# Kernel optimization log

Measured on AMD Instinct MI355X. Metric: run time of the kernel, lower is better.

The kernel has to match this reference:

```python
import jax, jax.numpy as jnp
import numpy as np

H = 56; W = 56; WS = 7; SHIFT = 3; HEADS = 6; C = 192
HD = C // HEADS; N = WS * WS; NWH = H // WS; NWW = W // WS; NW = NWH * NWW
MLP_HID = 4 * C
EPS = 1e-5


def _rel_index(ws):
    coords = np.stack(np.meshgrid(np.arange(ws), np.arange(ws), indexing='ij'))  # [2,ws,ws]
    cf = coords.reshape(2, -1)                       # [2,N]
    rc = (cf[:, :, None] - cf[:, None, :]).transpose(1, 2, 0).astype(np.int64)  # [N,N,2]
    rc[..., 0] += ws - 1
    rc[..., 1] += ws - 1
    rc[..., 0] *= 2 * ws - 1
    return rc.sum(-1)                                # [N,N]


def _attn_mask(h, w, ws, shift):
    img = np.zeros((h, w), dtype=np.float32)
    slices = (slice(0, -ws), slice(-ws, -shift), slice(-shift, None))
    cnt = 0
    for hs in slices:
        for wsl in slices:
            img[hs, wsl] = cnt
            cnt += 1
    mw = img.reshape(h // ws, ws, w // ws, ws).transpose(0, 2, 1, 3).reshape(-1, ws * ws)  # [nW,N]
    am = mw[:, None, :] - mw[:, :, None]             # [nW,N,N] (unsqueeze(1)-unsqueeze(2))
    return np.where(am != 0, np.float32(-100.0), np.float32(0.0))


REL_IDX = jnp.asarray(_rel_index(WS))
ATTN_MASK = jnp.asarray(_attn_mask(H, W, WS, SHIFT))


def _ln(x, w, b):
    m = jnp.mean(x, axis=-1, keepdims=True)
    v = jnp.mean((x - m) ** 2, axis=-1, keepdims=True)
    return (x - m) * jax.lax.rsqrt(v + EPS) * w + b


def setup_inputs() -> dict:
    key = jax.random.key(0)
    ks = jax.random.split(key, 8)
    B = 64
    s = 0.02
    return {
        'x': jax.random.normal(ks[0], (B, H * W, C), jnp.float32),
        'norm1_w': jnp.ones((C,), jnp.float32),
        'norm1_b': jnp.zeros((C,), jnp.float32),
        'qkv_w': jax.random.normal(ks[1], (C, 3 * C), jnp.float32) * s,
        'qkv_b': jnp.zeros((3 * C,), jnp.float32),
        'proj_w': jax.random.normal(ks[2], (C, C), jnp.float32) * s,
        'proj_b': jnp.zeros((C,), jnp.float32),
        'rel_bias': jax.random.normal(ks[3], ((2 * WS - 1) ** 2, HEADS), jnp.float32) * s,
        'norm2_w': jnp.ones((C,), jnp.float32),
        'norm2_b': jnp.zeros((C,), jnp.float32),
        'fc1_w': jax.random.normal(ks[4], (C, MLP_HID), jnp.float32) * s,
        'fc1_b': jnp.zeros((MLP_HID,), jnp.float32),
        'fc2_w': jax.random.normal(ks[5], (MLP_HID, C), jnp.float32) * s,
        'fc2_b': jnp.zeros((C,), jnp.float32),
    }


def reference(x, norm1_w, norm1_b, qkv_w, qkv_b, proj_w, proj_b, rel_bias,
              norm2_w, norm2_b, fc1_w, fc1_b, fc2_w, fc2_b):
    B = x.shape[0]
    shortcut = x
    h = _ln(x, norm1_w, norm1_b).reshape(B, H, W, C)
    h = jnp.roll(h, (-SHIFT, -SHIFT), axis=(1, 2))
    # window partition -> [B*nW, N, C]
    wx = h.reshape(B, NWH, WS, NWW, WS, C).transpose(0, 1, 3, 2, 4, 5).reshape(B * NW, N, C)
    qkv = (wx @ qkv_w + qkv_b).reshape(B * NW, N, 3, HEADS, HD).transpose(2, 0, 3, 1, 4)
    q, k, v = qkv[0], qkv[1], qkv[2]                 # [BnW, heads, N, hd]
    attn = jnp.einsum('bhnd,bhmd->bhnm', q, k) * (HD ** -0.5)
    bias = rel_bias[REL_IDX.reshape(-1)].reshape(N, N, HEADS).transpose(2, 0, 1)  # [heads,N,N]
    attn = attn + bias[None]
    attn = attn.reshape(B, NW, HEADS, N, N) + ATTN_MASK[None, :, None]
    attn = jax.nn.softmax(attn.reshape(B * NW, HEADS, N, N), axis=-1)
    out = jnp.einsum('bhnm,bhmd->bhnd', attn, v).transpose(0, 2, 1, 3).reshape(B * NW, N, C)
    out = out @ proj_w + proj_b
    # window reverse -> [B,H,W,C]
    out = out.reshape(B, NWH, NWW, WS, WS, C).transpose(0, 1, 3, 2, 4, 5).reshape(B, H, W, C)
    out = jnp.roll(out, (SHIFT, SHIFT), axis=(1, 2)).reshape(B, H * W, C)
    x = shortcut + out
    h2 = _ln(x, norm2_w, norm2_b)
    h2 = jax.nn.gelu(h2 @ fc1_w + fc1_b, approximate=False)
    h2 = h2 @ fc2_w + fc2_b
    return x + h2
```

## Files before the change

kernel.cpp:

```cpp
#include <hip/hip_runtime.h>
#include <hip/hip_bf16.h>
#include <math.h>

typedef __bf16 bf16;
typedef bf16  bf16x4 __attribute__((ext_vector_type(4)));
typedef bf16  bf16x8 __attribute__((ext_vector_type(8)));
typedef float f32x4  __attribute__((ext_vector_type(4)));

#define CD 192
#define NHEADS 6

__device__ __forceinline__ bf16x8 ld_frag(const bf16* p, int r0, int k0, int ld) {
  const int l = threadIdx.x & 63;
  return *reinterpret_cast<const bf16x8*>(p + (r0 + (l & 15)) * ld + (k0 + 8 * (l >> 4)));
}

__device__ __forceinline__ f32x4 mfma16(bf16x8 a, bf16x8 b, f32x4 c) {
  return __builtin_amdgcn_mfma_f32_16x16x32_bf16(a, b, c, 0, 0, 0);
}

__device__ __forceinline__ float gelu_f(float v) {
  const float e = __expf(-1.5957691216057308f * (v + 0.044715f * v * v * v));
  return v * __builtin_amdgcn_rcpf(1.f + e);
}

__global__ void prep_pack(const float* __restrict__ src, bf16* __restrict__ dst, int K, int N) {
  const int t = blockIdx.x * 256 + threadIdx.x;
  const int ktiles = K >> 5;
  const int total = (N >> 4) * ktiles * 64;
  if (t >= total) return;
  const int l  = t & 63;
  const int r  = t >> 6;
  const int kt = r % ktiles;
  const int ng = r / ktiles;
  const int n  = ng * 16 + (l & 15);
  const int k0 = kt * 32 + 8 * (l >> 4);
  bf16x8 v;
  #pragma unroll
  for (int j = 0; j < 8; ++j) v[j] = (bf16)src[(size_t)(k0 + j) * N + n];
  *(reinterpret_cast<bf16x8*>(dst) + t) = v;
}

__global__ void prep_bm(const float* __restrict__ relb, float* __restrict__ bm) {
  const int idx = blockIdx.x * 256 + threadIdx.x;
  if (idx >= 4 * 6 * 64 * 64) return;
  const int k = idx & 63;
  const int r = (idx >> 6) & 63;
  const int h = (idx >> 12) % 6;
  const int c = idx / (4096 * 6);
  float v = -3000.f;
  if (r < 49 && k < 49) {
    const int rh = r / 7, rw = r % 7, kh = k / 7, kw = k % 7;
    const int crh = (c & 2) ? (rh < 4 ? 1 : 2) : 0;
    const int crw = (c & 1) ? (rw < 4 ? 1 : 2) : 0;
    const int ckh = (c & 2) ? (kh < 4 ? 1 : 2) : 0;
    const int ckw = (c & 1) ? (kw < 4 ? 1 : 2) : 0;
    const float mask = (crh == ckh && crw == ckw) ? 0.f : -100.f;
    v = relb[((rh - kh + 6) * 13 + (rw - kw + 6)) * 6 + h] + mask;
  }
  bm[idx] = v;
}

__global__ __launch_bounds__(768, 1)
void swin_attn_kernel(const float* __restrict__ x,
                      const float* __restrict__ n1w, const float* __restrict__ n1b,
                      const bf16* __restrict__ wqf, const float* __restrict__ qkvb,
                      const bf16* __restrict__ wpf, const float* __restrict__ projb,
                      const float* __restrict__ bm,
                      float* __restrict__ out)
{
  __shared__ alignas(16) bf16 sQ[NHEADS][64 * 40];
  __shared__ alignas(16) bf16 sK[NHEADS][64 * 40];
  __shared__ alignas(16) bf16 sVT[NHEADS][32 * 72];
  __shared__ alignas(16) bf16 sU[NHEADS * 64 * 72];

  const int l    = threadIdx.x & 63;
  const int wv   = threadIdx.x >> 6;
  const int h    = wv >> 1;
  const int half = wv & 1;
  const int r0w  = half * 32;
  const int b  = blockIdx.x >> 6;
  const int wi = blockIdx.x & 63;
  const int wh = wi >> 3, ww = wi & 7;
  const int cw = ((wh == 7) ? 2 : 0) + ((ww == 7) ? 1 : 0);

  bf16* sA = sU;

  float xv0[5], xv1[5], xv2[5];
  size_t basea[5];
  {
    #pragma unroll
    for (int it = 0; it < 5; ++it) {
      const int t = wv + it * 12;
      if (t < 49) {
        const int th = t / 7, tw = t - 7 * th;
        const int ho = (wh * 7 + th + 3) % 56;
        const int wo = (ww * 7 + tw + 3) % 56;
        const size_t base = ((size_t)b * 3136 + ho * 56 + wo) * CD;
        basea[it] = base;
        xv0[it] = x[base + l]; xv1[it] = x[base + l + 64]; xv2[it] = x[base + l + 128];
      }
    }
    const float w0 = n1w[l], w1 = n1w[l + 64], w2 = n1w[l + 128];
    const float c0 = n1b[l], c1 = n1b[l + 64], c2 = n1b[l + 128];
    #pragma unroll
    for (int it = 0; it < 5; ++it) {
      const int t = wv + it * 12;
      if (t < 49) {
        const float v0 = xv0[it], v1 = xv1[it], v2 = xv2[it];
        float s  = v0 + v1 + v2;
        float ss = v0 * v0 + v1 * v1 + v2 * v2;
        #pragma unroll
        for (int off = 32; off; off >>= 1) { s += __shfl_xor(s, off); ss += __shfl_xor(ss, off); }
        const float mean = s * (1.f / 192.f);
        const float inv  = rsqrtf(ss * (1.f / 192.f) - mean * mean + 1e-5f);
        sA[t * 200 + l]       = (bf16)((v0 - mean) * inv * w0 + c0);
        sA[t * 200 + l + 64]  = (bf16)((v1 - mean) * inv * w1 + c1);
        sA[t * 200 + l + 128] = (bf16)((v2 - mean) * inv * w2 + c2);
      }
    }
    for (int i = threadIdx.x; i < 15 * 200; i += 768) sA[49 * 200 + i] = (bf16)0.f;
  }
  __syncthreads();

  float bmreg[2][4][4];
  {
    const float* bmb = bm + ((size_t)(cw * 6 + h) << 12) + (l & 15);
    #pragma unroll
    for (int mt = 0; mt < 2; ++mt)
      #pragma unroll
      for (int i = 0; i < 4; ++i) {
        const int r = r0w + mt * 16 + (l >> 4) * 4 + i;
        #pragma unroll
        for (int nt = 0; nt < 4; ++nt)
          bmreg[mt][i][nt] = bmb[r * 64 + nt * 16];
      }
  }

  {
    const bf16x8* bq = reinterpret_cast<const bf16x8*>(wqf) + l;
    const int cs = wv;
    f32x4 acc[3][4] = {};
    #pragma unroll
    for (int ks = 0; ks < 6; ++ks) {
      const int k0 = ks * 32;
      bf16x8 af[4];
      #pragma unroll
      for (int mt = 0; mt < 4; ++mt) af[mt] = ld_frag(sA, mt * 16, k0, 200);
      #pragma unroll
      for (int nt = 0; nt < 3; ++nt) {
        const bf16x8 bfr = bq[((cs * 3 + nt) * 6 + ks) * 64];
        #pragma unroll
        for (int mt = 0; mt < 4; ++mt) acc[nt][mt] = mfma16(af[mt], bfr, acc[nt][mt]);
      }
    }
    #pragma unroll
    for (int nt = 0; nt < 3; ++nt) {
      const int col0 = cs * 48 + nt * 16;
      const int which = col0 / 192;
      const int rem   = col0 - which * 192;
      const int hh    = rem >> 5;
      const int cc    = (rem & 31) + (l & 15);
      const float bias = qkvb[col0 + (l & 15)];
      #pragma unroll
      for (int mt = 0; mt < 4; ++mt) {
        const int rb = mt * 16 + (l >> 4) * 4;
        if (which == 2) {
          bf16x4 pv;
          #pragma unroll
          for (int i = 0; i < 4; ++i) pv[i] = (bf16)(acc[nt][mt][i] + bias);
          *reinterpret_cast<bf16x4*>(&sVT[hh][cc * 72 + rb]) = pv;
        } else if (which == 0) {
          #pragma unroll
          for (int i = 0; i < 4; ++i)
            sQ[hh][(rb + i) * 40 + cc] = (bf16)((acc[nt][mt][i] + bias) * 0.17677669529663689f);
        } else {
          #pragma unroll
          for (int i = 0; i < 4; ++i)
            sK[hh][(rb + i) * 40 + cc] = (bf16)(acc[nt][mt][i] + bias);
        }
      }
    }
  }
  __syncthreads();

  bf16* sP = sU + h * (64 * 72);
  {
    f32x4 sc[2][4] = {};
    bf16x8 qf0 = ld_frag(sQ[h], r0w,      0, 40);
    bf16x8 qf1 = ld_frag(sQ[h], r0w + 16, 0, 40);
    #pragma unroll
    for (int nt = 0; nt < 4; ++nt) {
      const bf16x8 kf = ld_frag(sK[h], nt * 16, 0, 40);
      sc[0][nt] = mfma16(qf0, kf, sc[0][nt]);
      sc[1][nt] = mfma16(qf1, kf, sc[1][nt]);
    }
    #pragma unroll
    for (int mt = 0; mt < 2; ++mt)
      #pragma unroll
      for (int i = 0; i < 4; ++i) {
        const int r = r0w + mt * 16 + (l >> 4) * 4 + i;
        float p[4], sum = 0.f;
        #pragma unroll
        for (int nt = 0; nt < 4; ++nt) {
          p[nt] = __expf(sc[mt][nt][i] + bmreg[mt][i][nt]);
          sum += p[nt];
        }
        #pragma unroll
        for (int off = 1; off < 16; off <<= 1) sum += __shfl_xor(sum, off);
        const float isum = __builtin_amdgcn_rcpf(sum);
        #pragma unroll
        for (int nt = 0; nt < 4; ++nt)
          sP[r * 72 + nt * 16 + (l & 15)] = (bf16)(p[nt] * isum);
      }
  }

  f32x4 o[2][2] = {};
  #pragma unroll
  for (int ks = 0; ks < 2; ++ks) {
    const int k0 = ks * 32;
    bf16x8 pf0 = ld_frag(sP, r0w,      k0, 72);
    bf16x8 pf1 = ld_frag(sP, r0w + 16, k0, 72);
    #pragma unroll
    for (int nt = 0; nt < 2; ++nt) {
      const bf16x8 vf = ld_frag(sVT[h], nt * 16, k0, 72);
      o[0][nt] = mfma16(pf0, vf, o[0][nt]);
      o[1][nt] = mfma16(pf1, vf, o[1][nt]);
    }
  }
  __syncthreads();
  {
    bf16* sAO = sU;
    #pragma unroll
    for (int nt = 0; nt < 2; ++nt) {
      const int c = h * 32 + nt * 16 + (l & 15);
      #pragma unroll
      for (int mt = 0; mt < 2; ++mt)
        #pragma unroll
        for (int i = 0; i < 4; ++i) {
          const int r = r0w + mt * 16 + (l >> 4) * 4 + i;
          sAO[r * 200 + c] = (bf16)o[mt][nt][i];
        }
    }
  }
  __syncthreads();

  f32x4 po[4] = {};
  {
    const bf16* sAO = sU;
    const bf16x8* bp = reinterpret_cast<const bf16x8*>(wpf) + l;
    #pragma unroll
    for (int ks = 0; ks < 6; ++ks) {
      const int k0 = ks * 32;
      const bf16x8 bfr = bp[(wv * 6 + ks) * 64];
      #pragma unroll
      for (int mt = 0; mt < 4; ++mt) {
        bf16x8 af = ld_frag(sAO, mt * 16, k0, 200);
        po[mt] = mfma16(af, bfr, po[mt]);
      }
    }
  }
  {
    bf16* sPO = &sVT[0][0];
    const int c = wv * 16 + (l & 15);
    const float bias = projb[c];
    #pragma unroll
    for (int mt = 0; mt < 4; ++mt)
      #pragma unroll
      for (int i = 0; i < 4; ++i) {
        const int r = mt * 16 + (l >> 4) * 4 + i;
        sPO[r * 200 + c] = (bf16)(po[mt][i] + bias);
      }
  }
  __syncthreads();

  {
    const bf16* sPO = &sVT[0][0];
    #pragma unroll
    for (int it = 0; it < 5; ++it) {
      const int r = wv + it * 12;
      if (r < 49) {
        const size_t base = basea[it];
        out[base + l]       = (float)sPO[r * 200 + l]       + xv0[it];
        out[base + l + 64]  = (float)sPO[r * 200 + l + 64]  + xv1[it];
        out[base + l + 128] = (float)sPO[r * 200 + l + 128] + xv2[it];
      }
    }
  }
}

__global__ __launch_bounds__(512, 6)
void swin_mlp_kernel(const float* __restrict__ n2w, const float* __restrict__ n2b,
                     const bf16* __restrict__ w1f, const float* __restrict__ fb1,
                     const bf16* __restrict__ w2f, const float* __restrict__ fb2,
                     float* __restrict__ io)
{
  __shared__ alignas(16) bf16 sA[64 * 200];
  __shared__ alignas(16) bf16 sH[2][64 * 72];
  const int l  = threadIdx.x & 63;
  const int wv = threadIdx.x >> 6;
  const int wr = wv & 1;
  const int wc = wv >> 1;
  const size_t t0 = (size_t)blockIdx.x * 64;

  {
    const float w0 = n2w[l], w1 = n2w[l + 64], w2 = n2w[l + 128];
    const float c0 = n2b[l], c1 = n2b[l + 64], c2 = n2b[l + 128];
    for (int t = wv; t < 64; t += 8) {
      const float* xr = io + (t0 + t) * CD;
      float v0 = xr[l], v1 = xr[l + 64], v2 = xr[l + 128];
      float s  = v0 + v1 + v2;
      float ss = v0 * v0 + v1 * v1 + v2 * v2;
      #pragma unroll
      for (int off = 32; off; off >>= 1) { s += __shfl_xor(s, off); ss += __shfl_xor(ss, off); }
      const float mean = s * (1.f / 192.f);
      const float inv  = rsqrtf(ss * (1.f / 192.f) - mean * mean + 1e-5f);
      sA[t * 200 + l]       = (bf16)((v0 - mean) * inv * w0 + c0);
      sA[t * 200 + l + 64]  = (bf16)((v1 - mean) * inv * w1 + c1);
      sA[t * 200 + l + 128] = (bf16)((v2 - mean) * inv * w2 + c2);
    }
  }
  __syncthreads();

  f32x4 oacc[2][3] = {};
  const bf16x8* w1p = reinterpret_cast<const bf16x8*>(w1f) + l;
  const bf16x8* w2p = reinterpret_cast<const bf16x8*>(w2f) + l;

  for (int kc = 0; kc < 12; ++kc) {
    bf16* hb = sH[kc & 1];
    f32x4 acc[2] = {};
    {
      bf16x8 b1[6];
      const bf16x8* b1p = w1p + ((kc * 4 + wc) * 6) * 64;
      #pragma unroll
      for (int ks = 0; ks < 6; ++ks) b1[ks] = b1p[ks * 64];

      #pragma unroll
      for (int ks = 0; ks < 6; ++ks) {
        const int k0 = ks * 32;
        bf16x8 af0 = ld_frag(sA, wr * 32,      k0, 200);
        bf16x8 af1 = ld_frag(sA, wr * 32 + 16, k0, 200);
        acc[0] = mfma16(af0, b1[ks], acc[0]);
        acc[1] = mfma16(af1, b1[ks], acc[1]);
      }
    }

    bf16x8 b2[6];
    #pragma unroll
    for (int ks = 0; ks < 2; ++ks)
      #pragma unroll
      for (int nt = 0; nt < 3; ++nt)
        b2[ks * 3 + nt] = w2p[((wc * 3 + nt) * 24 + kc * 2 + ks) * 64];

    {
      const int col = wc * 16 + (l & 15);
      const float bias = fb1[kc * 64 + col];
      #pragma unroll
      for (int mt = 0; mt < 2; ++mt)
        #pragma unroll
        for (int i = 0; i < 4; ++i) {
          const int r = wr * 32 + mt * 16 + (l >> 4) * 4 + i;
          hb[r * 72 + col] = (bf16)gelu_f(acc[mt][i] + bias);
        }
    }
    __syncthreads();
    #pragma unroll
    for (int ks = 0; ks < 2; ++ks) {
      const int k0 = ks * 32;
      bf16x8 af0 = ld_frag(hb, wr * 32,      k0, 72);
      bf16x8 af1 = ld_frag(hb, wr * 32 + 16, k0, 72);
      #pragma unroll
      for (int nt = 0; nt < 3; ++nt) {
        oacc[0][nt] = mfma16(af0, b2[ks * 3 + nt], oacc[0][nt]);
        oacc[1][nt] = mfma16(af1, b2[ks * 3 + nt], oacc[1][nt]);
      }
    }
  }

  #pragma unroll
  for (int nt = 0; nt < 3; ++nt) {
    const int col = wc * 48 + nt * 16 + (l & 15);
    const float bias = fb2[col];
    #pragma unroll
    for (int mt = 0; mt < 2; ++mt)
      #pragma unroll
      for (int i = 0; i < 4; ++i) {
        const int r = wr * 32 + mt * 16 + (l >> 4) * 4 + i;
        const size_t idx = (t0 + r) * CD + col;
        __builtin_nontemporal_store(oacc[mt][nt][i] + bias + io[idx], &io[idx]);
      }
  }
}

extern "C" void kernel_launch(void* const* d_in, const int* in_sizes, int n_in,
                              void* d_out, int out_size, void* d_ws, size_t ws_size,
                              hipStream_t stream) {
  const float* x     = (const float*)d_in[0];
  const float* n1w   = (const float*)d_in[1];
  const float* n1b   = (const float*)d_in[2];
  const float* qkvw  = (const float*)d_in[3];
  const float* qkvb  = (const float*)d_in[4];
  const float* projw = (const float*)d_in[5];
  const float* projb = (const float*)d_in[6];
  const float* relb  = (const float*)d_in[7];
  const float* n2w   = (const float*)d_in[8];
  const float* n2b   = (const float*)d_in[9];
  const float* f1w   = (const float*)d_in[10];
  const float* f1b   = (const float*)d_in[11];
  const float* f2w   = (const float*)d_in[12];
  const float* f2b   = (const float*)d_in[13];

  char* ws = (char*)d_ws;
  bf16*  wqf = (bf16*)(ws + 0);
  bf16*  wpf = (bf16*)(ws + 221184);
  bf16*  w1f = (bf16*)(ws + 294912);
  bf16*  w2f = (bf16*)(ws + 589824);
  float* bm  = (float*)(ws + 884736);

  prep_pack<<<(36 * 6 * 64 + 255) / 256, 256, 0, stream>>>(qkvw, wqf, 192, 576);
  prep_pack<<<(12 * 6 * 64 + 255) / 256, 256, 0, stream>>>(projw, wpf, 192, 192);
  prep_pack<<<(48 * 6 * 64 + 255) / 256, 256, 0, stream>>>(f1w, w1f, 192, 768);
  prep_pack<<<(12 * 24 * 64 + 255) / 256, 256, 0, stream>>>(f2w, w2f, 768, 192);
  prep_bm<<<(4 * 6 * 64 * 64 + 255) / 256, 256, 0, stream>>>(relb, bm);

  swin_attn_kernel<<<4096, 768, 0, stream>>>(x, n1w, n1b, wqf, qkvb, wpf, projb, bm, (float*)d_out);
  swin_mlp_kernel<<<3136, 512, 0, stream>>>(n2w, n2b, w1f, f1b, w2f, f2b, (float*)d_out);
}
```

Baseline: 470.1 us.

## Process two windows per attention block and prefetch both windows' inputs up front

New measurement: 814.9 us. 73.3% more time.

```diff
diff --git a/kernel.cpp b/kernel.cpp
--- a/kernel.cpp
+++ b/kernel.cpp
@@ -79,16 +79,20 @@
   const int h    = wv >> 1;
   const int half = wv & 1;
   const int r0w  = half * 32;
-  const int b  = blockIdx.x >> 6;
-  const int wi = blockIdx.x & 63;
-  const int wh = wi >> 3, ww = wi & 7;
-  const int cw = ((wh == 7) ? 2 : 0) + ((ww == 7) ? 1 : 0);
 
   bf16* sA = sU;
 
-  float xv0[5], xv1[5], xv2[5];
-  size_t basea[5];
-  {
+  int whA[2], wwA[2], cwA[2];
+  float xv0[2][5], xv1[2][5], xv2[2][5];
+  size_t basea[2][5];
+  #pragma unroll
+  for (int w2 = 0; w2 < 2; ++w2) {
+    const int w  = blockIdx.x * 2 + w2;
+    const int b  = w >> 6;
+    const int wi = w & 63;
+    const int wh = wi >> 3, ww = wi & 7;
+    whA[w2] = wh; wwA[w2] = ww;
+    cwA[w2] = ((wh == 7) ? 2 : 0) + ((ww == 7) ? 1 : 0);
     #pragma unroll
     for (int it = 0; it < 5; ++it) {
       const int t = wv + it * 12;
@@ -97,17 +101,27 @@
         const int ho = (wh * 7 + th + 3) % 56;
         const int wo = (ww * 7 + tw + 3) % 56;
         const size_t base = ((size_t)b * 3136 + ho * 56 + wo) * CD;
-        basea[it] = base;
-        xv0[it] = x[base + l]; xv1[it] = x[base + l + 64]; xv2[it] = x[base + l + 128];
-      }
-    }
-    const float w0 = n1w[l], w1 = n1w[l + 64], w2 = n1w[l + 128];
-    const float c0 = n1b[l], c1 = n1b[l + 64], c2 = n1b[l + 128];
+        basea[w2][it] = base;
+        xv0[w2][it] = x[base + l];
+        xv1[w2][it] = x[base + l + 64];
+        xv2[w2][it] = x[base + l + 128];
+      }
+    }
+  }
+
+  const float w0 = n1w[l], w1 = n1w[l + 64], w2c = n1w[l + 128];
+  const float c0 = n1b[l], c1 = n1b[l + 64], c2 = n1b[l + 128];
+  const bf16x8* bq = reinterpret_cast<const bf16x8*>(wqf) + l;
+  const bf16x8* bp = reinterpret_cast<const bf16x8*>(wpf) + l;
+
+  for (int w2 = 0; w2 < 2; ++w2) {
+    const int cw = cwA[w2];
+
     #pragma unroll
     for (int it = 0; it < 5; ++it) {
       const int t = wv + it * 12;
       if (t < 49) {
-        const float v0 = xv0[it], v1 = xv1[it], v2 = xv2[it];
+        const float v0 = xv0[w2][it], v1 = xv1[w2][it], v2 = xv2[w2][it];
         float s  = v0 + v1 + v2;
         float ss = v0 * v0 + v1 * v1 + v2 * v2;
         #pragma unroll
@@ -116,174 +130,172 @@
         const float inv  = rsqrtf(ss * (1.f / 192.f) - mean * mean + 1e-5f);
         sA[t * 200 + l]       = (bf16)((v0 - mean) * inv * w0 + c0);
         sA[t * 200 + l + 64]  = (bf16)((v1 - mean) * inv * w1 + c1);
-        sA[t * 200 + l + 128] = (bf16)((v2 - mean) * inv * w2 + c2);
+        sA[t * 200 + l + 128] = (bf16)((v2 - mean) * inv * w2c + c2);
       }
     }
     for (int i = threadIdx.x; i < 15 * 200; i += 768) sA[49 * 200 + i] = (bf16)0.f;
-  }
-  __syncthreads();
-
-  float bmreg[2][4][4];
-  {
-    const float* bmb = bm + ((size_t)(cw * 6 + h) << 12) + (l & 15);
-    #pragma unroll
-    for (int mt = 0; mt < 2; ++mt)
-      #pragma unroll
-      for (int i = 0; i < 4; ++i) {
-        const int r = r0w + mt * 16 + (l >> 4) * 4 + i;
-        #pragma unroll
-        for (int nt = 0; nt < 4; ++nt)
-          bmreg[mt][i][nt] = bmb[r * 64 + nt * 16];
-      }
-  }
-
-  {
-    const bf16x8* bq = reinterpret_cast<const bf16x8*>(wqf) + l;
-    const int cs = wv;
-    f32x4 acc[3][4] = {};
-    #pragma unroll
-    for (int ks = 0; ks < 6; ++ks) {
-      const int k0 = ks * 32;
-      bf16x8 af[4];
-      #pragma unroll
-      for (int mt = 0; mt < 4; ++mt) af[mt] = ld_frag(sA, mt * 16, k0, 200);
-      #pragma unroll
-      for (int nt = 0; nt < 3; ++nt) {
-        const bf16x8 bfr = bq[((cs * 3 + nt) * 6 + ks) * 64];
-        #pragma unroll
-        for (int mt = 0; mt < 4; ++mt) acc[nt][mt] = mfma16(af[mt], bfr, acc[nt][mt]);
-      }
-    }
-    #pragma unroll
-    for (int nt = 0; nt < 3; ++nt) {
-      const int col0 = cs * 48 + nt * 16;
-      const int which = col0 / 192;
-      const int rem   = col0 - which * 192;
-      const int hh    = rem >> 5;
-      const int cc    = (rem & 31) + (l & 15);
-      const float bias = qkvb[col0 + (l & 15)];
-      #pragma unroll
-      for (int mt = 0; mt < 4; ++mt) {
-        const int rb = mt * 16 + (l >> 4) * 4;
-        if (which == 2) {
-          bf16x4 pv;
-          #pragma unroll
-          for (int i = 0; i < 4; ++i) pv[i] = (bf16)(acc[nt][mt][i] + bias);
-          *reinterpret_cast<bf16x4*>(&sVT[hh][cc * 72 + rb]) = pv;
-        } else if (which == 0) {
-          #pragma unroll
-          for (int i = 0; i < 4; ++i)
-            sQ[hh][(rb + i) * 40 + cc] = (bf16)((acc[nt][mt][i] + bias) * 0.17677669529663689f);
-        } else {
-          #pragma unroll
-          for (int i = 0; i < 4; ++i)
-            sK[hh][(rb + i) * 40 + cc] = (bf16)(acc[nt][mt][i] + bias);
-        }
-      }
-    }
-  }
-  __syncthreads();
-
-  bf16* sP = sU + h * (64 * 72);
-  {
-    f32x4 sc[2][4] = {};
-    bf16x8 qf0 = ld_frag(sQ[h], r0w,      0, 40);
-    bf16x8 qf1 = ld_frag(sQ[h], r0w + 16, 0, 40);
-    #pragma unroll
-    for (int nt = 0; nt < 4; ++nt) {
-      const bf16x8 kf = ld_frag(sK[h], nt * 16, 0, 40);
-      sc[0][nt] = mfma16(qf0, kf, sc[0][nt]);
-      sc[1][nt] = mfma16(qf1, kf, sc[1][nt]);
-    }
-    #pragma unroll
-    for (int mt = 0; mt < 2; ++mt)
-      #pragma unroll
-      for (int i = 0; i < 4; ++i) {
-        const int r = r0w + mt * 16 + (l >> 4) * 4 + i;
-        float p[4], sum = 0.f;
-        #pragma unroll
-        for (int nt = 0; nt < 4; ++nt) {
-          p[nt] = __expf(sc[mt][nt][i] + bmreg[mt][i][nt]);
-          sum += p[nt];
-        }
-        #pragma unroll
-        for (int off = 1; off < 16; off <<= 1) sum += __shfl_xor(sum, off);
-        const float isum = __builtin_amdgcn_rcpf(sum);
-        #pragma unroll
-        for (int nt = 0; nt < 4; ++nt)
-          sP[r * 72 + nt * 16 + (l & 15)] = (bf16)(p[nt] * isum);
-      }
-  }
-
-  f32x4 o[2][2] = {};
-  #pragma unroll
-  for (int ks = 0; ks < 2; ++ks) {
-    const int k0 = ks * 32;
-    bf16x8 pf0 = ld_frag(sP, r0w,      k0, 72);
-    bf16x8 pf1 = ld_frag(sP, r0w + 16, k0, 72);
-    #pragma unroll
-    for (int nt = 0; nt < 2; ++nt) {
-      const bf16x8 vf = ld_frag(sVT[h], nt * 16, k0, 72);
-      o[0][nt] = mfma16(pf0, vf, o[0][nt]);
-      o[1][nt] = mfma16(pf1, vf, o[1][nt]);
-    }
-  }
-  __syncthreads();
-  {
-    bf16* sAO = sU;
-    #pragma unroll
-    for (int nt = 0; nt < 2; ++nt) {
-      const int c = h * 32 + nt * 16 + (l & 15);
+    __syncthreads();
+
+    float bmreg[2][4][4];
+    {
+      const float* bmb = bm + ((size_t)(cw * 6 + h) << 12) + (l & 15);
       #pragma unroll
       for (int mt = 0; mt < 2; ++mt)
         #pragma unroll
         for (int i = 0; i < 4; ++i) {
           const int r = r0w + mt * 16 + (l >> 4) * 4 + i;
-          sAO[r * 200 + c] = (bf16)o[mt][nt][i];
-        }
-    }
-  }
-  __syncthreads();
-
-  f32x4 po[4] = {};
-  {
-    const bf16* sAO = sU;
-    const bf16x8* bp = reinterpret_cast<const bf16x8*>(wpf) + l;
-    #pragma unroll
-    for (int ks = 0; ks < 6; ++ks) {
+          #pragma unroll
+          for (int nt = 0; nt < 4; ++nt)
+            bmreg[mt][i][nt] = bmb[r * 64 + nt * 16];
+        }
+    }
+
+    {
+      const int cs = wv;
+      f32x4 acc[3][4] = {};
+      #pragma unroll
+      for (int ks = 0; ks < 6; ++ks) {
+        const int k0 = ks * 32;
+        bf16x8 af[4];
+        #pragma unroll
+        for (int mt = 0; mt < 4; ++mt) af[mt] = ld_frag(sA, mt * 16, k0, 200);
+        #pragma unroll
+        for (int nt = 0; nt < 3; ++nt) {
+          const bf16x8 bfr = bq[((cs * 3 + nt) * 6 + ks) * 64];
+          #pragma unroll
+          for (int mt = 0; mt < 4; ++mt) acc[nt][mt] = mfma16(af[mt], bfr, acc[nt][mt]);
+        }
+      }
+      #pragma unroll
+      for (int nt = 0; nt < 3; ++nt) {
+        const int col0 = cs * 48 + nt * 16;
+        const int which = col0 / 192;
+        const int rem   = col0 - which * 192;
+        const int hh    = rem >> 5;
+        const int cc    = (rem & 31) + (l & 15);
+        const float bias = qkvb[col0 + (l & 15)];
+        #pragma unroll
+        for (int mt = 0; mt < 4; ++mt) {
+          const int rb = mt * 16 + (l >> 4) * 4;
+          if (which == 2) {
+            bf16x4 pv;
+            #pragma unroll
+            for (int i = 0; i < 4; ++i) pv[i] = (bf16)(acc[nt][mt][i] + bias);
+            *reinterpret_cast<bf16x4*>(&sVT[hh][cc * 72 + rb]) = pv;
+          } else if (which == 0) {
+            #pragma unroll
+            for (int i = 0; i < 4; ++i)
+              sQ[hh][(rb + i) * 40 + cc] = (bf16)((acc[nt][mt][i] + bias) * 0.17677669529663689f);
+          } else {
+            #pragma unroll
+            for (int i = 0; i < 4; ++i)
+              sK[hh][(rb + i) * 40 + cc] = (bf16)(acc[nt][mt][i] + bias);
+          }
+        }
+      }
+    }
+    __syncthreads();
+
+    bf16* sP = sU + h * (64 * 72);
+    {
+      f32x4 sc[2][4] = {};
+      bf16x8 qf0 = ld_frag(sQ[h], r0w,      0, 40);
+      bf16x8 qf1 = ld_frag(sQ[h], r0w + 16, 0, 40);
+      #pragma unroll
+      for (int nt = 0; nt < 4; ++nt) {
+        const bf16x8 kf = ld_frag(sK[h], nt * 16, 0, 40);
+        sc[0][nt] = mfma16(qf0, kf, sc[0][nt]);
+        sc[1][nt] = mfma16(qf1, kf, sc[1][nt]);
+      }
+      #pragma unroll
+      for (int mt = 0; mt < 2; ++mt)
+        #pragma unroll
+        for (int i = 0; i < 4; ++i) {
+          const int r = r0w + mt * 16 + (l >> 4) * 4 + i;
+          float p[4], sum = 0.f;
+          #pragma unroll
+          for (int nt = 0; nt < 4; ++nt) {
+            p[nt] = __expf(sc[mt][nt][i] + bmreg[mt][i][nt]);
+            sum += p[nt];
+          }
+          #pragma unroll
+          for (int off = 1; off < 16; off <<= 1) sum += __shfl_xor(sum, off);
+          const float isum = __builtin_amdgcn_rcpf(sum);
+          #pragma unroll
+          for (int nt = 0; nt < 4; ++nt)
+            sP[r * 72 + nt * 16 + (l & 15)] = (bf16)(p[nt] * isum);
+        }
+    }
+
+    f32x4 o[2][2] = {};
+    #pragma unroll
+    for (int ks = 0; ks < 2; ++ks) {
       const int k0 = ks * 32;
-      const bf16x8 bfr = bp[(wv * 6 + ks) * 64];
-      #pragma unroll
-      for (int mt = 0; mt < 4; ++mt) {
-        bf16x8 af = ld_frag(sAO, mt * 16, k0, 200);
-        po[mt] = mfma16(af, bfr, po[mt]);
-      }
-    }
-  }
-  {
-    bf16* sPO = &sVT[0][0];
-    const int c = wv * 16 + (l & 15);
-    const float bias = projb[c];
-    #pragma unroll
-    for (int mt = 0; mt < 4; ++mt)
-      #pragma unroll
-      for (int i = 0; i < 4; ++i) {
-        const int r = mt * 16 + (l >> 4) * 4 + i;
-        sPO[r * 200 + c] = (bf16)(po[mt][i] + bias);
-      }
-  }
-  __syncthreads();
-
-  {
-    const bf16* sPO = &sVT[0][0];
-    #pragma unroll
-    for (int it = 0; it < 5; ++it) {
-      const int r = wv + it * 12;
-      if (r < 49) {
-        const size_t base = basea[it];
-        out[base + l]       = (float)sPO[r * 200 + l]       + xv0[it];
-        out[base + l + 64]  = (float)sPO[r * 200 + l + 64]  + xv1[it];
-        out[base + l + 128] = (float)sPO[r * 200 + l + 128] + xv2[it];
+      bf16x8 pf0 = ld_frag(sP, r0w,      k0, 72);
+      bf16x8 pf1 = ld_frag(sP, r0w + 16, k0, 72);
+      #pragma unroll
+      for (int nt = 0; nt < 2; ++nt) {
+        const bf16x8 vf = ld_frag(sVT[h], nt * 16, k0, 72);
+        o[0][nt] = mfma16(pf0, vf, o[0][nt]);
+        o[1][nt] = mfma16(pf1, vf, o[1][nt]);
+      }
+    }
+    __syncthreads();
+    {
+      bf16* sAO = sU;
+      #pragma unroll
+      for (int nt = 0; nt < 2; ++nt) {
+        const int c = h * 32 + nt * 16 + (l & 15);
+        #pragma unroll
+        for (int mt = 0; mt < 2; ++mt)
+          #pragma unroll
+          for (int i = 0; i < 4; ++i) {
+            const int r = r0w + mt * 16 + (l >> 4) * 4 + i;
+            sAO[r * 200 + c] = (bf16)o[mt][nt][i];
+          }
+      }
+    }
+    __syncthreads();
+
+    f32x4 po[4] = {};
+    {
+      const bf16* sAO = sU;
+      #pragma unroll
+      for (int ks = 0; ks < 6; ++ks) {
+        const int k0 = ks * 32;
+        const bf16x8 bfr = bp[(wv * 6 + ks) * 64];
+        #pragma unroll
+        for (int mt = 0; mt < 4; ++mt) {
+          bf16x8 af = ld_frag(sAO, mt * 16, k0, 200);
+          po[mt] = mfma16(af, bfr, po[mt]);
+        }
+      }
+    }
+    {
+      bf16* sPO = &sVT[0][0];
+      const int c = wv * 16 + (l & 15);
+      const float bias = projb[c];
+      #pragma unroll
+      for (int mt = 0; mt < 4; ++mt)
+        #pragma unroll
+        for (int i = 0; i < 4; ++i) {
+          const int r = mt * 16 + (l >> 4) * 4 + i;
+          sPO[r * 200 + c] = (bf16)(po[mt][i] + bias);
+        }
+    }
+    __syncthreads();
+
+    {
+      const bf16* sPO = &sVT[0][0];
+      #pragma unroll
+      for (int it = 0; it < 5; ++it) {
+        const int r = wv + it * 12;
+        if (r < 49) {
+          const size_t base = basea[w2][it];
+          out[base + l]       = (float)sPO[r * 200 + l]       + xv0[w2][it];
+          out[base + l + 64]  = (float)sPO[r * 200 + l + 64]  + xv1[w2][it];
+          out[base + l + 128] = (float)sPO[r * 200 + l + 128] + xv2[w2][it];
+        }
       }
     }
   }
@@ -423,6 +435,6 @@
   prep_pack<<<(12 * 24 * 64 + 255) / 256, 256, 0, stream>>>(f2w, w2f, 768, 192);
   prep_bm<<<(4 * 6 * 64 * 64 + 255) / 256, 256, 0, stream>>>(relb, bm);
 
-  swin_attn_kernel<<<4096, 768, 0, stream>>>(x, n1w, n1b, wqf, qkvb, wpf, projb, bm, (float*)d_out);
+  swin_attn_kernel<<<2048, 768, 0, stream>>>(x, n1w, n1b, wqf, qkvb, wpf, projb, bm, (float*)d_out);
   swin_mlp_kernel<<<3136, 512, 0, stream>>>(n2w, n2b, w1f, f1b, w2f, f2b, (float*)d_out);
 }
```
